# Optimization experiments

Measured on AMD Instinct MI355X. Metric: run time of the kernel, lower is better.

Reference implementation:

```python
import jax, jax.numpy as jnp
import numpy as np

M, N, DIM, BATCH = 64, 64, 256, 4096
GRID = M * N
ALPHA = 0.5
SIGMA = float(np.sqrt(M * N) / 2.0)  # 32.0, default sigma


def _grid_locations():
    ii, jj = np.meshgrid(np.arange(M), np.arange(N), indexing='ij')
    return np.stack([ii.ravel(), jj.ravel()], axis=1).astype(np.int64)  # [GRID, 2]


def _grid_distance_mat(locs):
    # non-periodic: squared euclidean distance between grid locations
    d = locs[:, None, :].astype(np.float32) - locs[None, :, :].astype(np.float32)
    return (d ** 2).sum(-1).astype(np.float32)  # [GRID, GRID]


def setup_inputs() -> dict:
    key = jax.random.key(0)
    k1, k2 = jax.random.split(key)
    locs = _grid_locations()
    return {
        'x': jax.random.normal(k1, (BATCH, DIM), dtype=jnp.float32),
        'centroids': jax.random.normal(k2, (GRID, DIM), dtype=jnp.float32),
        'distance_mat': jnp.asarray(_grid_distance_mat(locs)),
        'locations': jnp.asarray(locs),
        'learning_rate_op': jnp.ones((), dtype=jnp.float32),
    }


def reference(x, centroids, distance_mat, locations, learning_rate_op):
    B = x.shape[0]
    # cdist(x, centroids) with p=2: [B, GRID]
    d2 = ((x ** 2).sum(-1, keepdims=True)
          + (centroids ** 2).sum(-1)[None, :]
          - 2.0 * x @ centroids.T)
    dists = jnp.sqrt(jnp.maximum(d2, 0.0))
    bmu_index = jnp.argmin(dists, axis=-1)            # [B]
    mindist = jnp.min(dists, axis=-1)                 # [B]
    bmu_loc = locations[bmu_index]                    # [B, 2]

    alpha_op = ALPHA * learning_rate_op
    sigma_op = SIGMA * learning_rate_op
    bmu_dist_sq = distance_mat[bmu_index]             # gather rows: [B, GRID]
    neighbourhood = jnp.exp(-bmu_dist_sq / (2.0 * sigma_op ** 2 + 1e-5))
    lrm = alpha_op * neighbourhood                    # [B, GRID]

    # delta = mean_b lrm[b,g] * (x[b,d] - centroids[g,d]), factored to avoid [B,GRID,DIM]
    delta = (lrm.T @ x) / B - jnp.mean(lrm, axis=0)[:, None] * centroids
    new_centroids = centroids + delta
    return new_centroids, bmu_loc, jnp.mean(mindist)
```

## Files before the change

### kernel.cpp

```cpp
#include <hip/hip_runtime.h>
#include <cstdint>
#include <cstddef>

#define DIM    256
#define BATCH  4096
#define GRID_N 4096
#define STEPS  12

typedef _Float16 f16x8 __attribute__((ext_vector_type(8)));
typedef _Float16 f16x4 __attribute__((ext_vector_type(4)));
typedef float    f32x4 __attribute__((ext_vector_type(4)));

#define OFF_APK  0u
#define OFF_S    0u
#define OFF_BPK  1048576u
#define OFF_CNT  1048576u
#define OFF_U    1052672u
#define OFF_GX   2101248u
#define OFF_WCNT 2105344u
#define OFF_XN   2109440u
#define OFF_CN   2113536u
#define OFF_MD   2117632u
#define OFF_PV   2121728u
#define OFF_PI   2252800u

#define OUT_BMU  1048576u
#define OUT_MD   1056768u

__device__ __forceinline__ void load_lds16(const void* g, void* l) {
  __builtin_amdgcn_global_load_lds(
      (const __attribute__((address_space(1))) unsigned int*)g,
      (__attribute__((address_space(3))) unsigned int*)l, 16, 0, 0);
}

__global__ __launch_bounds__(256) void packnorm_kernel(
    const float* __restrict__ x, const float* __restrict__ cen,
    const float* __restrict__ lr,
    _Float16* __restrict__ Apk, _Float16* __restrict__ Bpk,
    float* __restrict__ xn, float* __restrict__ cn, float* __restrict__ Gx) {
  int row  = blockIdx.x * 4 + (threadIdx.x >> 6);
  int lane = threadIdx.x & 63;
  bool isx = row < BATCH;
  const float* src = isx ? (x + (size_t)row * DIM)
                         : (cen + (size_t)(row - BATCH) * DIM);
  float4 v = *(const float4*)(src + lane * 4);

  _Float16 h0 = (_Float16)v.x, h1 = (_Float16)v.y,
           h2 = (_Float16)v.z, h3 = (_Float16)v.w;
  _Float16 l0 = (_Float16)(v.x - (float)h0), l1 = (_Float16)(v.y - (float)h1),
           l2 = (_Float16)(v.z - (float)h2), l3 = (_Float16)(v.w - (float)h3);

  _Float16* dst = (isx ? Apk : Bpk) + (size_t)(isx ? row : row - BATCH) * 512;
  *(f16x4*)(dst + lane * 4)       = (f16x4){h0, h1, h2, h3};
  *(f16x4*)(dst + 256 + lane * 4) = (f16x4){l0, l1, l2, l3};

  float s = v.x * v.x + v.y * v.y + v.z * v.z + v.w * v.w;
#pragma unroll
  for (int off = 32; off >= 1; off >>= 1) s += __shfl_xor(s, off);
  if (lane == 0) {
    if (isx) xn[row] = s;
    else     cn[row - BATCH] = s;
  }

  if (blockIdx.x == 0) {
    float sg  = 32.f * lr[0];
    float inv = 1.f / (2.f * sg * sg + 1e-5f);
#pragma unroll
    for (int i = 0; i < 16; ++i) {
      int g = i * 256 + threadIdx.x;
      float d = (float)((g >> 6) - (g & 63));
      Gx[g] = expf(-d * d * inv);
    }
  }
}

__global__ __launch_bounds__(256) void gemm_argmin_kernel(
    const _Float16* __restrict__ Apk, const _Float16* __restrict__ Bpk,
    const float* __restrict__ cnorm, float* __restrict__ pv, int* __restrict__ pi) {
  __shared__ __align__(16) _Float16 lds[2][2][8192];
  const int tid  = threadIdx.x;
  const int lane = tid & 63, w = tid >> 6;
  const int wr = w >> 1, wc = w & 1;
  const int row0 = blockIdx.y * 128, col0 = blockIdx.x * 128;
  const int t15 = lane & 15, q = lane >> 4;
  const int sw  = t15 & 7;
  const int srow   = w * 32 + (lane >> 3);
  const int schunk = (lane & 7) ^ ((lane >> 3) & 7);

  f32x4 acc[4][4];
#pragma unroll
  for (int m = 0; m < 4; ++m)
#pragma unroll
    for (int n = 0; n < 4; ++n) acc[m][n] = (f32x4){0.f, 0.f, 0.f, 0.f};

  auto STAGE = [&](int b, int step) {
    const int seg = step >> 2, k = (step & 3) << 6;
    const int aoff = ((seg == 2) ? 256 : 0) + k;
    const int boff = ((seg == 1) ? 256 : 0) + k;
    const _Float16* Ab = Apk + (size_t)(row0 + srow) * 512 + aoff + schunk * 8;
    const _Float16* Bb = Bpk + (size_t)(col0 + srow) * 512 + boff + schunk * 8;
    _Float16* Al = &lds[b][0][w * 2048];
    _Float16* Bl = &lds[b][1][w * 2048];
#pragma unroll
    for (int i = 0; i < 4; ++i) {
      load_lds16(Ab + (size_t)i * 8 * 512, Al + i * 512);
      load_lds16(Bb + (size_t)i * 8 * 512, Bl + i * 512);
    }
  };

  STAGE(0, 0);
  for (int t = 0; t < STEPS; ++t) {
    const int b = t & 1;
    __syncthreads();
    if (t + 1 < STEPS) STAGE(b ^ 1, t + 1);
#pragma unroll
    for (int kk = 0; kk < 2; ++kk) {
      f16x8 af[4], bf[4];
#pragma unroll
      for (int m = 0; m < 4; ++m) {
        int r = wr * 64 + m * 16 + t15;
        af[m] = *(const f16x8*)&lds[b][0][r * 64 + (((kk * 4 + q) ^ sw) * 8)];
      }
#pragma unroll
      for (int n = 0; n < 4; ++n) {
        int r = wc * 64 + n * 16 + t15;
        bf[n] = *(const f16x8*)&lds[b][1][r * 64 + (((kk * 4 + q) ^ sw) * 8)];
      }
#pragma unroll
      for (int m = 0; m < 4; ++m)
#pragma unroll
        for (int n = 0; n < 4; ++n)
          acc[m][n] = __builtin_amdgcn_mfma_f32_16x16x32_f16(af[m], bf[n], acc[m][n], 0, 0, 0);
    }
  }
  __syncthreads();

  float cnv[4];
#pragma unroll
  for (int n = 0; n < 4; ++n) cnv[n] = cnorm[col0 + wc * 64 + n * 16 + t15];

  float* cv = (float*)&lds[0][0][0];
  int*   ci = (int*)&lds[0][1][0];
#pragma unroll
  for (int m = 0; m < 4; ++m) {
#pragma unroll
    for (int reg = 0; reg < 4; ++reg) {
      float bv = 1e30f; int bi = 0x7fffffff;
#pragma unroll
      for (int n = 0; n < 4; ++n) {
        float v = cnv[n] - 2.f * acc[m][n][reg];
        if (v < bv) { bv = v; bi = col0 + wc * 64 + n * 16 + t15; }
      }
#pragma unroll
      for (int off = 1; off < 16; off <<= 1) {
        float ov = __shfl_xor(bv, off);
        int   oi = __shfl_xor(bi, off);
        if (ov < bv || (ov == bv && oi < bi)) { bv = ov; bi = oi; }
      }
      if (t15 == 0) {
        int r = wr * 64 + m * 16 + q * 4 + reg;
        cv[r * 2 + wc] = bv;
        ci[r * 2 + wc] = bi;
      }
    }
  }
  __syncthreads();
  if (tid < 128) {
    float v0 = cv[tid * 2];     int i0 = ci[tid * 2];
    float v1 = cv[tid * 2 + 1]; int i1 = ci[tid * 2 + 1];
    if (v1 < v0 || (v1 == v0 && i1 < i0)) { v0 = v1; i0 = i1; }
    pv[(size_t)(row0 + tid) * 32 + blockIdx.x] = v0;
    pi[(size_t)(row0 + tid) * 32 + blockIdx.x] = i0;
  }
}

__global__ __launch_bounds__(256) void finalize_kernel(
    const float* __restrict__ pv, const int* __restrict__ pi,
    const float* __restrict__ xn, const float* __restrict__ x,
    float* __restrict__ S, float* __restrict__ cnt,
    float* __restrict__ md, float* __restrict__ out) {
  const int w = threadIdx.x >> 6, l = threadIdx.x & 63;
  const int b = blockIdx.x * 4 + w;
  float v = pv[(size_t)b * 32 + (l & 31)];
  int idx  = pi[(size_t)b * 32 + (l & 31)];
#pragma unroll
  for (int off = 16; off >= 1; off >>= 1) {
    float ov = __shfl_xor(v, off);
    int   oi = __shfl_xor(idx, off);
    if (ov < v || (ov == v && oi < idx)) { v = ov; idx = oi; }
  }
  if (l == 0) {
    md[b] = sqrtf(fmaxf(xn[b] + v, 0.f));
    out[OUT_BMU + (size_t)b * 2 + 0] = (float)(idx >> 6);
    out[OUT_BMU + (size_t)b * 2 + 1] = (float)(idx & 63);
    atomicAdd(cnt + idx, 1.f);
  }
#pragma unroll
  for (int c = 0; c < 4; ++c)
    atomicAdd(S + (size_t)idx * DIM + c * 64 + l, x[(size_t)b * DIM + c * 64 + l]);
}

__global__ __launch_bounds__(256) void wcnt_kernel(const float* __restrict__ cnt,
                                                   const float* __restrict__ Gx,
                                                   const float* __restrict__ md,
                                                   float* __restrict__ Wcnt,
                                                   float* __restrict__ out) {
  __shared__ float cs[4096], gs[4096], inner[4096];
  const int t = threadIdx.x;
  for (int i = 0; i < 16; i++) { cs[i * 256 + t] = cnt[i * 256 + t]; gs[i * 256 + t] = Gx[i * 256 + t]; }
  __syncthreads();
  for (int i = 0; i < 16; i++) {
    int idx = i * 256 + t; int ki = idx >> 6, gj = idx & 63;
    float a = 0.f;
    for (int kj = 0; kj < 64; kj++) a += gs[kj * 64 + gj] * cs[ki * 64 + kj];
    inner[idx] = a;
  }
  __syncthreads();
  const int g = blockIdx.x * 256 + t, gi = g >> 6, gj = g & 63;
  float a = 0.f;
  for (int ki = 0; ki < 64; ki++) a += gs[gi * 64 + ki] * inner[ki * 64 + gj];
  Wcnt[g] = a;

  if (blockIdx.x == 0) {
    float s = 0.f;
#pragma unroll
    for (int i = 0; i < 16; i++) s += md[i * 256 + t];
#pragma unroll
    for (int off = 32; off >= 1; off >>= 1) s += __shfl_xor(s, off);
    __shared__ float wsum[4];
    if ((t & 63) == 0) wsum[t >> 6] = s;
    __syncthreads();
    if (t == 0) out[OUT_MD] = (wsum[0] + wsum[1] + wsum[2] + wsum[3]) * (1.f / (float)BATCH);
  }
}

__global__ __launch_bounds__(256) void e1_kernel(const float* __restrict__ S,
                                                 const float* __restrict__ Gx,
                                                 float* __restrict__ U) {
  __shared__ float Ss[4096];
  const int t = threadIdx.x, dd = t & 63, gq = t >> 6;
  const int kj = blockIdx.x >> 2, dq = blockIdx.x & 3;
#pragma unroll 4
  for (int i = 0; i < 16; ++i) {
    int ki = i * 4 + gq;
    Ss[ki * 64 + dd] = S[((size_t)ki * 64 + kj) * 256 + dq * 64 + dd];
  }
  __syncthreads();
  float a[16];
#pragma unroll
  for (int gg = 0; gg < 16; ++gg) a[gg] = 0.f;
  for (int ki = 0; ki < 64; ++ki) {
    float s = Ss[ki * 64 + dd];
#pragma unroll
    for (int gg = 0; gg < 16; ++gg)
      a[gg] += Gx[ki * 64 + gq * 16 + gg] * s;
  }
#pragma unroll
  for (int gg = 0; gg < 16; ++gg)
    U[((size_t)(gq * 16 + gg) * 64 + kj) * 256 + dq * 64 + dd] = a[gg];
}

__global__ __launch_bounds__(256) void e2_kernel(const float* __restrict__ U,
                                                 const float* __restrict__ Gx,
                                                 const float* __restrict__ Wcnt,
                                                 const float* __restrict__ cen,
                                                 const float* __restrict__ lr,
                                                 float* __restrict__ out) {
  __shared__ float Us[4096];
  const int t = threadIdx.x, dd = t & 63, gq = t >> 6;
  const int gi = blockIdx.x >> 2, dq = blockIdx.x & 3;
#pragma unroll 4
  for (int i = 0; i < 16; ++i) {
    int kj = i * 4 + gq;
    Us[kj * 64 + dd] = U[((size_t)gi * 64 + kj) * 256 + dq * 64 + dd];
  }
  __syncthreads();
  float a[16];
#pragma unroll
  for (int gg = 0; gg < 16; ++gg) a[gg] = 0.f;
  for (int kj = 0; kj < 64; ++kj) {
    float s = Us[kj * 64 + dd];
#pragma unroll
    for (int gg = 0; gg < 16; ++gg)
      a[gg] += Gx[kj * 64 + gq * 16 + gg] * s;
  }
  const float coef = 0.5f * lr[0] / (float)BATCH;
#pragma unroll
  for (int gg = 0; gg < 16; ++gg) {
    int g = gi * 64 + gq * 16 + gg;
    float c = cen[(size_t)g * 256 + dq * 64 + dd];
    out[(size_t)g * 256 + dq * 64 + dd] = c + coef * (a[gg] - Wcnt[g] * c);
  }
}

extern "C" void kernel_launch(void* const* d_in, const int* in_sizes, int n_in,
                              void* d_out, int out_size, void* d_ws, size_t ws_size,
                              hipStream_t stream) {
  const float* x   = (const float*)d_in[0];
  const float* cen = (const float*)d_in[1];
  const float* lr  = (const float*)d_in[4];
  float* out = (float*)d_out;
  float* ws  = (float*)d_ws;

  _Float16* Apk = (_Float16*)(ws + OFF_APK);
  _Float16* Bpk = (_Float16*)(ws + OFF_BPK);
  float* S    = ws + OFF_S;
  float* cnt  = ws + OFF_CNT;
  float* U    = ws + OFF_U;
  float* Gx   = ws + OFF_GX;
  float* Wcnt = ws + OFF_WCNT;
  float* xn   = ws + OFF_XN;
  float* cnw  = ws + OFF_CN;
  float* md   = ws + OFF_MD;
  float* pv   = ws + OFF_PV;
  int*   pi   = (int*)(ws + OFF_PI);

  packnorm_kernel<<<2048, 256, 0, stream>>>(x, cen, lr, Apk, Bpk, xn, cnw, Gx);
  gemm_argmin_kernel<<<dim3(32, 32), 256, 0, stream>>>(Apk, Bpk, cnw, pv, pi);
  hipMemsetAsync(S, 0, (size_t)(1048576 + 4096) * sizeof(float), stream);
  finalize_kernel<<<1024, 256, 0, stream>>>(pv, pi, xn, x, S, cnt, md, out);
  wcnt_kernel<<<16, 256, 0, stream>>>(cnt, Gx, md, Wcnt, out);
  e1_kernel<<<256, 256, 0, stream>>>(S, Gx, U);
  e2_kernel<<<256, 256, 0, stream>>>(U, Gx, Wcnt, cen, lr, out);
}
```

Measured before the change: 187.3 us.

## Fuse all SOM stages into one cooperative persistent kernel with grid syncs

Replaces the chain of six kernel launches and a memset with a single cooperative kernel of 512 blocks that runs packing, the fp16-split GEMM with argmin, zeroing, scatter-accumulation, the separable neighbourhood passes and the final update, separated by grid.sync barriers. Each block now handles several tiles that previously took separate blocks. The aim is to remove launch gaps and the memset. The cost is that 512 blocks give less parallelism in the GEMM phase than the 1024-block grid did, and the grid barriers add overhead. If the cooperative launch fails, it falls back to the old multi-kernel path.

```diff
diff --git a/kernel.cpp b/kernel.cpp
--- a/kernel.cpp
+++ b/kernel.cpp
@@ -1,10 +1,12 @@
 #include <hip/hip_runtime.h>
+#include <hip/hip_cooperative_groups.h>
 #include <cstdint>
 #include <cstddef>
 
+namespace cg = cooperative_groups;
+
 #define DIM    256
 #define BATCH  4096
-#define GRID_N 4096
 #define STEPS  12
 
 typedef _Float16 f16x8 __attribute__((ext_vector_type(8)));
@@ -14,15 +16,15 @@
 #define OFF_APK  0u
 #define OFF_S    0u
 #define OFF_BPK  1048576u
-#define OFF_CNT  1048576u
-#define OFF_U    1052672u
-#define OFF_GX   2101248u
-#define OFF_WCNT 2105344u
-#define OFF_XN   2109440u
-#define OFF_CN   2113536u
-#define OFF_MD   2117632u
-#define OFF_PV   2121728u
-#define OFF_PI   2252800u
+#define OFF_U    1048576u
+#define OFF_GX   2097152u
+#define OFF_XN   2101248u
+#define OFF_CN   2105344u
+#define OFF_MD   2109440u
+#define OFF_WCNT 2113536u
+#define OFF_PV   2117632u
+#define OFF_PI   2248704u
+#define OFF_CNT  2379776u
 
 #define OUT_BMU  1048576u
 #define OUT_MD   1056768u
@@ -31,6 +33,285 @@
   __builtin_amdgcn_global_load_lds(
       (const __attribute__((address_space(1))) unsigned int*)g,
       (__attribute__((address_space(3))) unsigned int*)l, 16, 0, 0);
+}
+
+__global__ __launch_bounds__(256, 2) void som_mega(
+    const float* __restrict__ x, const float* __restrict__ cen,
+    const float* __restrict__ lr, float* __restrict__ ws,
+    float* __restrict__ out) {
+  cg::grid_group grid = cg::this_grid();
+  __shared__ __align__(16) unsigned char smem[65536];
+
+  const int bid  = blockIdx.x;
+  const int tid  = threadIdx.x;
+  const int lane = tid & 63;
+  const int w    = tid >> 6;
+
+  _Float16* Apk = (_Float16*)(ws + OFF_APK);
+  _Float16* Bpk = (_Float16*)(ws + OFF_BPK);
+  float* S    = ws + OFF_S;
+  float* U    = ws + OFF_U;
+  float* Gx   = ws + OFF_GX;
+  float* xn   = ws + OFF_XN;
+  float* cnw  = ws + OFF_CN;
+  float* md   = ws + OFF_MD;
+  float* Wcnt = ws + OFF_WCNT;
+  float* pv   = ws + OFF_PV;
+  int*   pi   = (int*)(ws + OFF_PI);
+  float* cnt  = ws + OFF_CNT;
+
+  {
+#pragma unroll
+    for (int pass = 0; pass < 4; ++pass) {
+      int row = bid * 16 + pass * 4 + w;
+      bool isx = row < BATCH;
+      const float* src = isx ? (x + (size_t)row * DIM)
+                             : (cen + (size_t)(row - BATCH) * DIM);
+      float4 v = *(const float4*)(src + lane * 4);
+      _Float16 h0 = (_Float16)v.x, h1 = (_Float16)v.y,
+               h2 = (_Float16)v.z, h3 = (_Float16)v.w;
+      _Float16 l0 = (_Float16)(v.x - (float)h0), l1 = (_Float16)(v.y - (float)h1),
+               l2 = (_Float16)(v.z - (float)h2), l3 = (_Float16)(v.w - (float)h3);
+      _Float16* dst = (isx ? Apk : Bpk) + (size_t)(isx ? row : row - BATCH) * 512;
+      *(f16x4*)(dst + lane * 4)       = (f16x4){h0, h1, h2, h3};
+      *(f16x4*)(dst + 256 + lane * 4) = (f16x4){l0, l1, l2, l3};
+      float s = v.x * v.x + v.y * v.y + v.z * v.z + v.w * v.w;
+#pragma unroll
+      for (int off = 32; off >= 1; off >>= 1) s += __shfl_xor(s, off);
+      if (lane == 0) { if (isx) xn[row] = s; else cnw[row - BATCH] = s; }
+    }
+    if (bid == 0) {
+      float sg  = 32.f * lr[0];
+      float inv = 1.f / (2.f * sg * sg + 1e-5f);
+#pragma unroll
+      for (int i = 0; i < 16; ++i) {
+        int g = i * 256 + tid;
+        float d = (float)((g >> 6) - (g & 63));
+        Gx[g] = expf(-d * d * inv);
+      }
+    } else if (bid == 1) {
+      float4 z = {0.f, 0.f, 0.f, 0.f};
+#pragma unroll
+      for (int i = 0; i < 4; ++i) ((float4*)cnt)[i * 256 + tid] = z;
+    }
+  }
+  grid.sync();
+
+  {
+    auto lds = (_Float16(*)[2][8192])smem;
+    const int wr = w >> 1, wc = w & 1;
+    const int by = bid >> 4, bxp = bid & 15;
+    const int row0 = by * 128;
+    const int t15 = lane & 15, q = lane >> 4;
+    const int swz = t15 & 7;
+    const int srow = w * 32 + (lane >> 3);
+    const int schunk = (lane & 7) ^ ((lane >> 3) & 7);
+
+    for (int tt = 0; tt < 2; ++tt) {
+      const int bx = bxp * 2 + tt;
+      const int col0 = bx * 128;
+      f32x4 acc[4][4];
+#pragma unroll
+      for (int m = 0; m < 4; ++m)
+#pragma unroll
+        for (int n = 0; n < 4; ++n) acc[m][n] = (f32x4){0.f, 0.f, 0.f, 0.f};
+
+      auto STAGE = [&](int b, int step) {
+        const int seg = step >> 2, k = (step & 3) << 6;
+        const int aoff = ((seg == 2) ? 256 : 0) + k;
+        const int boff = ((seg == 1) ? 256 : 0) + k;
+        const _Float16* Ab = Apk + (size_t)(row0 + srow) * 512 + aoff + schunk * 8;
+        const _Float16* Bb = Bpk + (size_t)(col0 + srow) * 512 + boff + schunk * 8;
+        _Float16* Al = &lds[b][0][w * 2048];
+        _Float16* Bl = &lds[b][1][w * 2048];
+#pragma unroll
+        for (int i = 0; i < 4; ++i) {
+          load_lds16(Ab + (size_t)i * 8 * 512, Al + i * 512);
+          load_lds16(Bb + (size_t)i * 8 * 512, Bl + i * 512);
+        }
+      };
+
+      STAGE(0, 0);
+      for (int t = 0; t < STEPS; ++t) {
+        const int b = t & 1;
+        __syncthreads();
+        if (t + 1 < STEPS) STAGE(b ^ 1, t + 1);
+#pragma unroll
+        for (int kk = 0; kk < 2; ++kk) {
+          f16x8 af[4], bf[4];
+#pragma unroll
+          for (int m = 0; m < 4; ++m) {
+            int r = wr * 64 + m * 16 + t15;
+            af[m] = *(const f16x8*)&lds[b][0][r * 64 + (((kk * 4 + q) ^ swz) * 8)];
+          }
+#pragma unroll
+          for (int n = 0; n < 4; ++n) {
+            int r = wc * 64 + n * 16 + t15;
+            bf[n] = *(const f16x8*)&lds[b][1][r * 64 + (((kk * 4 + q) ^ swz) * 8)];
+          }
+#pragma unroll
+          for (int m = 0; m < 4; ++m)
+#pragma unroll
+            for (int n = 0; n < 4; ++n)
+              acc[m][n] = __builtin_amdgcn_mfma_f32_16x16x32_f16(af[m], bf[n], acc[m][n], 0, 0, 0);
+        }
+      }
+      __syncthreads();
+
+      float cnv[4];
+#pragma unroll
+      for (int n = 0; n < 4; ++n) cnv[n] = cnw[col0 + wc * 64 + n * 16 + t15];
+
+      float* cv = (float*)smem;
+      int*   ci = (int*)(smem + 16384);
+#pragma unroll
+      for (int m = 0; m < 4; ++m) {
+#pragma unroll
+        for (int reg = 0; reg < 4; ++reg) {
+          float bv = 1e30f; int bi = 0x7fffffff;
+#pragma unroll
+          for (int n = 0; n < 4; ++n) {
+            float v = cnv[n] - 2.f * acc[m][n][reg];
+            if (v < bv) { bv = v; bi = col0 + wc * 64 + n * 16 + t15; }
+          }
+#pragma unroll
+          for (int off = 1; off < 16; off <<= 1) {
+            float ov = __shfl_xor(bv, off);
+            int   oi = __shfl_xor(bi, off);
+            if (ov < bv || (ov == bv && oi < bi)) { bv = ov; bi = oi; }
+          }
+          if (t15 == 0) {
+            int r = wr * 64 + m * 16 + q * 4 + reg;
+            cv[r * 2 + wc] = bv;
+            ci[r * 2 + wc] = bi;
+          }
+        }
+      }
+      __syncthreads();
+      if (tid < 128) {
+        float v0 = cv[tid * 2];     int i0 = ci[tid * 2];
+        float v1 = cv[tid * 2 + 1]; int i1 = ci[tid * 2 + 1];
+        if (v1 < v0 || (v1 == v0 && i1 < i0)) { v0 = v1; i0 = i1; }
+        pv[(size_t)(row0 + tid) * 32 + bx] = v0;
+        pi[(size_t)(row0 + tid) * 32 + bx] = i0;
+      }
+      __syncthreads();
+    }
+  }
+  grid.sync();
+
+  {
+    float4 z = {0.f, 0.f, 0.f, 0.f};
+    float4* S4 = (float4*)S;
+    S4[bid * 512 + tid] = z;
+    S4[bid * 512 + 256 + tid] = z;
+  }
+  grid.sync();
+
+  {
+#pragma unroll
+    for (int i = 0; i < 2; ++i) {
+      int b = bid * 8 + w * 2 + i;
+      float v = pv[(size_t)b * 32 + (lane & 31)];
+      int idx  = pi[(size_t)b * 32 + (lane & 31)];
+#pragma unroll
+      for (int off = 16; off >= 1; off >>= 1) {
+        float ov = __shfl_xor(v, off);
+        int   oi = __shfl_xor(idx, off);
+        if (ov < v || (ov == v && oi < idx)) { v = ov; idx = oi; }
+      }
+      if (lane == 0) {
+        md[b] = sqrtf(fmaxf(xn[b] + v, 0.f));
+        out[OUT_BMU + (size_t)b * 2 + 0] = (float)(idx >> 6);
+        out[OUT_BMU + (size_t)b * 2 + 1] = (float)(idx & 63);
+        atomicAdd(cnt + idx, 1.f);
+      }
+#pragma unroll
+      for (int c = 0; c < 4; ++c)
+        atomicAdd(S + (size_t)idx * DIM + c * 64 + lane,
+                  x[(size_t)b * DIM + c * 64 + lane]);
+    }
+  }
+  grid.sync();
+
+  if (bid < 256) {
+    float* Ss = (float*)smem;
+    const int dd = lane, gq = w;
+    const int kj = bid >> 2, dq = bid & 3;
+    for (int i = 0; i < 16; ++i) {
+      int ki = i * 4 + gq;
+      Ss[ki * 64 + dd] = S[((size_t)ki * 64 + kj) * 256 + dq * 64 + dd];
+    }
+    __syncthreads();
+    float a[16];
+#pragma unroll
+    for (int gg = 0; gg < 16; ++gg) a[gg] = 0.f;
+    for (int ki = 0; ki < 64; ++ki) {
+      float s = Ss[ki * 64 + dd];
+#pragma unroll
+      for (int gg = 0; gg < 16; ++gg)
+        a[gg] += Gx[ki * 64 + gq * 16 + gg] * s;
+    }
+#pragma unroll
+    for (int gg = 0; gg < 16; ++gg)
+      U[((size_t)(gq * 16 + gg) * 64 + kj) * 256 + dq * 64 + dd] = a[gg];
+  } else if (bid < 272) {
+    float* cs = (float*)smem;
+    float* gs = cs + 4096;
+    float* inner = gs + 4096;
+    const int t = tid;
+    for (int i = 0; i < 16; i++) { cs[i * 256 + t] = cnt[i * 256 + t]; gs[i * 256 + t] = Gx[i * 256 + t]; }
+    __syncthreads();
+    for (int i = 0; i < 16; i++) {
+      int idx = i * 256 + t; int ki = idx >> 6, gj = idx & 63;
+      float a = 0.f;
+      for (int kj2 = 0; kj2 < 64; kj2++) a += gs[kj2 * 64 + gj] * cs[ki * 64 + kj2];
+      inner[idx] = a;
+    }
+    __syncthreads();
+    const int g = (bid - 256) * 256 + t, gi = g >> 6, gj = g & 63;
+    float a = 0.f;
+    for (int ki = 0; ki < 64; ki++) a += gs[gi * 64 + ki] * inner[ki * 64 + gj];
+    Wcnt[g] = a;
+  } else if (bid == 272) {
+    float s = 0.f;
+#pragma unroll
+    for (int i = 0; i < 16; i++) s += md[i * 256 + tid];
+#pragma unroll
+    for (int off = 32; off >= 1; off >>= 1) s += __shfl_xor(s, off);
+    float* wsum = (float*)smem;
+    if (lane == 0) wsum[w] = s;
+    __syncthreads();
+    if (tid == 0) out[OUT_MD] = (wsum[0] + wsum[1] + wsum[2] + wsum[3]) * (1.f / (float)BATCH);
+  }
+  grid.sync();
+
+  if (bid < 256) {
+    float* Us = (float*)smem;
+    const int dd = lane, gq = w;
+    const int gi = bid >> 2, dq = bid & 3;
+    for (int i = 0; i < 16; ++i) {
+      int kj = i * 4 + gq;
+      Us[kj * 64 + dd] = U[((size_t)gi * 64 + kj) * 256 + dq * 64 + dd];
+    }
+    __syncthreads();
+    float a[16];
+#pragma unroll
+    for (int gg = 0; gg < 16; ++gg) a[gg] = 0.f;
+    for (int kj = 0; kj < 64; ++kj) {
+      float s = Us[kj * 64 + dd];
+#pragma unroll
+      for (int gg = 0; gg < 16; ++gg)
+        a[gg] += Gx[kj * 64 + gq * 16 + gg] * s;
+    }
+    const float coef = 0.5f * lr[0] / (float)BATCH;
+#pragma unroll
+    for (int gg = 0; gg < 16; ++gg) {
+      int g = gi * 64 + gq * 16 + gg;
+      float c = cen[(size_t)g * 256 + dq * 64 + dd];
+      out[(size_t)g * 256 + dq * 64 + dd] = c + coef * (a[gg] - Wcnt[g] * c);
+    }
+  }
 }
 
 __global__ __launch_bounds__(256) void packnorm_kernel(
@@ -44,24 +325,17 @@
   const float* src = isx ? (x + (size_t)row * DIM)
                          : (cen + (size_t)(row - BATCH) * DIM);
   float4 v = *(const float4*)(src + lane * 4);
-
   _Float16 h0 = (_Float16)v.x, h1 = (_Float16)v.y,
            h2 = (_Float16)v.z, h3 = (_Float16)v.w;
   _Float16 l0 = (_Float16)(v.x - (float)h0), l1 = (_Float16)(v.y - (float)h1),
            l2 = (_Float16)(v.z - (float)h2), l3 = (_Float16)(v.w - (float)h3);
-
   _Float16* dst = (isx ? Apk : Bpk) + (size_t)(isx ? row : row - BATCH) * 512;
   *(f16x4*)(dst + lane * 4)       = (f16x4){h0, h1, h2, h3};
   *(f16x4*)(dst + 256 + lane * 4) = (f16x4){l0, l1, l2, l3};
-
   float s = v.x * v.x + v.y * v.y + v.z * v.z + v.w * v.w;
 #pragma unroll
   for (int off = 32; off >= 1; off >>= 1) s += __shfl_xor(s, off);
-  if (lane == 0) {
-    if (isx) xn[row] = s;
-    else     cn[row - BATCH] = s;
-  }
-
+  if (lane == 0) { if (isx) xn[row] = s; else cn[row - BATCH] = s; }
   if (blockIdx.x == 0) {
     float sg  = 32.f * lr[0];
     float inv = 1.f / (2.f * sg * sg + 1e-5f);
@@ -220,7 +494,6 @@
   float a = 0.f;
   for (int ki = 0; ki < 64; ki++) a += gs[gi * 64 + ki] * inner[ki * 64 + gj];
   Wcnt[g] = a;
-
   if (blockIdx.x == 0) {
     float s = 0.f;
 #pragma unroll
@@ -305,21 +578,27 @@
   _Float16* Apk = (_Float16*)(ws + OFF_APK);
   _Float16* Bpk = (_Float16*)(ws + OFF_BPK);
   float* S    = ws + OFF_S;
-  float* cnt  = ws + OFF_CNT;
   float* U    = ws + OFF_U;
   float* Gx   = ws + OFF_GX;
-  float* Wcnt = ws + OFF_WCNT;
   float* xn   = ws + OFF_XN;
   float* cnw  = ws + OFF_CN;
   float* md   = ws + OFF_MD;
+  float* Wcnt = ws + OFF_WCNT;
   float* pv   = ws + OFF_PV;
   int*   pi   = (int*)(ws + OFF_PI);
-
-  packnorm_kernel<<<2048, 256, 0, stream>>>(x, cen, lr, Apk, Bpk, xn, cnw, Gx);
-  gemm_argmin_kernel<<<dim3(32, 32), 256, 0, stream>>>(Apk, Bpk, cnw, pv, pi);
-  hipMemsetAsync(S, 0, (size_t)(1048576 + 4096) * sizeof(float), stream);
-  finalize_kernel<<<1024, 256, 0, stream>>>(pv, pi, xn, x, S, cnt, md, out);
-  wcnt_kernel<<<16, 256, 0, stream>>>(cnt, Gx, md, Wcnt, out);
-  e1_kernel<<<256, 256, 0, stream>>>(S, Gx, U);
-  e2_kernel<<<256, 256, 0, stream>>>(U, Gx, Wcnt, cen, lr, out);
-}
+  float* cnt  = ws + OFF_CNT;
+
+  void* args[] = { (void*)&x, (void*)&cen, (void*)&lr, (void*)&ws, (void*)&out };
+  hipError_t err = hipLaunchCooperativeKernel((const void*)som_mega, dim3(512),
+                                              dim3(256), args, 0, stream);
+  if (err != hipSuccess) {
+    packnorm_kernel<<<2048, 256, 0, stream>>>(x, cen, lr, Apk, Bpk, xn, cnw, Gx);
+    gemm_argmin_kernel<<<dim3(32, 32), 256, 0, stream>>>(Apk, Bpk, cnw, pv, pi);
+    hipMemsetAsync(S, 0, (size_t)1048576 * sizeof(float), stream);
+    hipMemsetAsync(cnt, 0, (size_t)4096 * sizeof(float), stream);
+    finalize_kernel<<<1024, 256, 0, stream>>>(pv, pi, xn, x, S, cnt, md, out);
+    wcnt_kernel<<<16, 256, 0, stream>>>(cnt, Gx, md, Wcnt, out);
+    e1_kernel<<<256, 256, 0, stream>>>(S, Gx, U);
+    e2_kernel<<<256, 256, 0, stream>>>(U, Gx, Wcnt, cen, lr, out);
+  }
+}
```

Result: slower. 481.7 us (+157.2%).

## Fuse wcnt into e1 launch and single-buffer GEMM LDS staging

Applied to the files above, without the earlier changes.

Merges the wcnt kernel and the mean-distance reduction into the e1 kernel as extra blocks (273 blocks total), removing one launch and letting the small Wcnt work run concurrently with the U computation. Separately, the GEMM argmin kernel drops LDS double buffering: each step now loads a tile, syncs, then computes, halving LDS use to raise occupancy. The cost is that global-to-LDS loads no longer overlap MFMA work within a block, and the e1 launch now mixes blocks of very different shape and shared-memory size, which may reduce its occupancy.

```diff
diff --git a/kernel.cpp b/kernel.cpp
--- a/kernel.cpp
+++ b/kernel.cpp
@@ -4,7 +4,6 @@
 
 #define DIM    256
 #define BATCH  4096
-#define GRID_N 4096
 #define STEPS  12
 
 typedef _Float16 f16x8 __attribute__((ext_vector_type(8)));
@@ -44,24 +43,17 @@
   const float* src = isx ? (x + (size_t)row * DIM)
                          : (cen + (size_t)(row - BATCH) * DIM);
   float4 v = *(const float4*)(src + lane * 4);
-
   _Float16 h0 = (_Float16)v.x, h1 = (_Float16)v.y,
            h2 = (_Float16)v.z, h3 = (_Float16)v.w;
   _Float16 l0 = (_Float16)(v.x - (float)h0), l1 = (_Float16)(v.y - (float)h1),
            l2 = (_Float16)(v.z - (float)h2), l3 = (_Float16)(v.w - (float)h3);
-
   _Float16* dst = (isx ? Apk : Bpk) + (size_t)(isx ? row : row - BATCH) * 512;
   *(f16x4*)(dst + lane * 4)       = (f16x4){h0, h1, h2, h3};
   *(f16x4*)(dst + 256 + lane * 4) = (f16x4){l0, l1, l2, l3};
-
   float s = v.x * v.x + v.y * v.y + v.z * v.z + v.w * v.w;
 #pragma unroll
   for (int off = 32; off >= 1; off >>= 1) s += __shfl_xor(s, off);
-  if (lane == 0) {
-    if (isx) xn[row] = s;
-    else     cn[row - BATCH] = s;
-  }
-
+  if (lane == 0) { if (isx) xn[row] = s; else cn[row - BATCH] = s; }
   if (blockIdx.x == 0) {
     float sg  = 32.f * lr[0];
     float inv = 1.f / (2.f * sg * sg + 1e-5f);
@@ -77,7 +69,7 @@
 __global__ __launch_bounds__(256) void gemm_argmin_kernel(
     const _Float16* __restrict__ Apk, const _Float16* __restrict__ Bpk,
     const float* __restrict__ cnorm, float* __restrict__ pv, int* __restrict__ pi) {
-  __shared__ __align__(16) _Float16 lds[2][2][8192];
+  __shared__ __align__(16) _Float16 lds[2][8192];
   const int tid  = threadIdx.x;
   const int lane = tid & 63, w = tid >> 6;
   const int wr = w >> 1, wc = w & 1;
@@ -93,38 +85,35 @@
 #pragma unroll
     for (int n = 0; n < 4; ++n) acc[m][n] = (f32x4){0.f, 0.f, 0.f, 0.f};
 
-  auto STAGE = [&](int b, int step) {
-    const int seg = step >> 2, k = (step & 3) << 6;
-    const int aoff = ((seg == 2) ? 256 : 0) + k;
-    const int boff = ((seg == 1) ? 256 : 0) + k;
-    const _Float16* Ab = Apk + (size_t)(row0 + srow) * 512 + aoff + schunk * 8;
-    const _Float16* Bb = Bpk + (size_t)(col0 + srow) * 512 + boff + schunk * 8;
-    _Float16* Al = &lds[b][0][w * 2048];
-    _Float16* Bl = &lds[b][1][w * 2048];
-#pragma unroll
-    for (int i = 0; i < 4; ++i) {
-      load_lds16(Ab + (size_t)i * 8 * 512, Al + i * 512);
-      load_lds16(Bb + (size_t)i * 8 * 512, Bl + i * 512);
-    }
-  };
-
-  STAGE(0, 0);
   for (int t = 0; t < STEPS; ++t) {
-    const int b = t & 1;
-    __syncthreads();
-    if (t + 1 < STEPS) STAGE(b ^ 1, t + 1);
+    if (t) __syncthreads();
+    {
+      const int seg = t >> 2, k = (t & 3) << 6;
+      const int aoff = ((seg == 2) ? 256 : 0) + k;
+      const int boff = ((seg == 1) ? 256 : 0) + k;
+      const _Float16* Ab = Apk + (size_t)(row0 + srow) * 512 + aoff + schunk * 8;
+      const _Float16* Bb = Bpk + (size_t)(col0 + srow) * 512 + boff + schunk * 8;
+      _Float16* Al = &lds[0][w * 2048];
+      _Float16* Bl = &lds[1][w * 2048];
+#pragma unroll
+      for (int i = 0; i < 4; ++i) {
+        load_lds16(Ab + (size_t)i * 8 * 512, Al + i * 512);
+        load_lds16(Bb + (size_t)i * 8 * 512, Bl + i * 512);
+      }
+    }
+    __syncthreads();
 #pragma unroll
     for (int kk = 0; kk < 2; ++kk) {
       f16x8 af[4], bf[4];
 #pragma unroll
       for (int m = 0; m < 4; ++m) {
         int r = wr * 64 + m * 16 + t15;
-        af[m] = *(const f16x8*)&lds[b][0][r * 64 + (((kk * 4 + q) ^ sw) * 8)];
+        af[m] = *(const f16x8*)&lds[0][r * 64 + (((kk * 4 + q) ^ sw) * 8)];
       }
 #pragma unroll
       for (int n = 0; n < 4; ++n) {
         int r = wc * 64 + n * 16 + t15;
-        bf[n] = *(const f16x8*)&lds[b][1][r * 64 + (((kk * 4 + q) ^ sw) * 8)];
+        bf[n] = *(const f16x8*)&lds[1][r * 64 + (((kk * 4 + q) ^ sw) * 8)];
       }
 #pragma unroll
       for (int m = 0; m < 4; ++m)
@@ -139,8 +128,8 @@
 #pragma unroll
   for (int n = 0; n < 4; ++n) cnv[n] = cnorm[col0 + wc * 64 + n * 16 + t15];
 
-  float* cv = (float*)&lds[0][0][0];
-  int*   ci = (int*)&lds[0][1][0];
+  float* cv = (float*)&lds[0][0];
+  int*   ci = (int*)&lds[1][0];
 #pragma unroll
   for (int m = 0; m < 4; ++m) {
 #pragma unroll
@@ -200,64 +189,64 @@
     atomicAdd(S + (size_t)idx * DIM + c * 64 + l, x[(size_t)b * DIM + c * 64 + l]);
 }
 
-__global__ __launch_bounds__(256) void wcnt_kernel(const float* __restrict__ cnt,
-                                                   const float* __restrict__ Gx,
-                                                   const float* __restrict__ md,
-                                                   float* __restrict__ Wcnt,
-                                                   float* __restrict__ out) {
-  __shared__ float cs[4096], gs[4096], inner[4096];
-  const int t = threadIdx.x;
-  for (int i = 0; i < 16; i++) { cs[i * 256 + t] = cnt[i * 256 + t]; gs[i * 256 + t] = Gx[i * 256 + t]; }
-  __syncthreads();
-  for (int i = 0; i < 16; i++) {
-    int idx = i * 256 + t; int ki = idx >> 6, gj = idx & 63;
-    float a = 0.f;
-    for (int kj = 0; kj < 64; kj++) a += gs[kj * 64 + gj] * cs[ki * 64 + kj];
-    inner[idx] = a;
-  }
-  __syncthreads();
-  const int g = blockIdx.x * 256 + t, gi = g >> 6, gj = g & 63;
-  float a = 0.f;
-  for (int ki = 0; ki < 64; ki++) a += gs[gi * 64 + ki] * inner[ki * 64 + gj];
-  Wcnt[g] = a;
-
-  if (blockIdx.x == 0) {
-    float s = 0.f;
-#pragma unroll
-    for (int i = 0; i < 16; i++) s += md[i * 256 + t];
-#pragma unroll
-    for (int off = 32; off >= 1; off >>= 1) s += __shfl_xor(s, off);
-    __shared__ float wsum[4];
-    if ((t & 63) == 0) wsum[t >> 6] = s;
-    __syncthreads();
-    if (t == 0) out[OUT_MD] = (wsum[0] + wsum[1] + wsum[2] + wsum[3]) * (1.f / (float)BATCH);
-  }
-}
-
 __global__ __launch_bounds__(256) void e1_kernel(const float* __restrict__ S,
                                                  const float* __restrict__ Gx,
-                                                 float* __restrict__ U) {
-  __shared__ float Ss[4096];
-  const int t = threadIdx.x, dd = t & 63, gq = t >> 6;
-  const int kj = blockIdx.x >> 2, dq = blockIdx.x & 3;
+                                                 const float* __restrict__ cnt,
+                                                 const float* __restrict__ md,
+                                                 float* __restrict__ U,
+                                                 float* __restrict__ Wcnt,
+                                                 float* __restrict__ out) {
+  __shared__ float smem[12288];
+  const int bid = blockIdx.x, tid = threadIdx.x;
+  if (bid < 256) {
+    float* Ss = smem;
+    const int dd = tid & 63, gq = tid >> 6;
+    const int kj = bid >> 2, dq = bid & 3;
 #pragma unroll 4
-  for (int i = 0; i < 16; ++i) {
-    int ki = i * 4 + gq;
-    Ss[ki * 64 + dd] = S[((size_t)ki * 64 + kj) * 256 + dq * 64 + dd];
-  }
-  __syncthreads();
-  float a[16];
-#pragma unroll
-  for (int gg = 0; gg < 16; ++gg) a[gg] = 0.f;
-  for (int ki = 0; ki < 64; ++ki) {
-    float s = Ss[ki * 64 + dd];
+    for (int i = 0; i < 16; ++i) {
+      int ki = i * 4 + gq;
+      Ss[ki * 64 + dd] = S[((size_t)ki * 64 + kj) * 256 + dq * 64 + dd];
+    }
+    __syncthreads();
+    float a[16];
+#pragma unroll
+    for (int gg = 0; gg < 16; ++gg) a[gg] = 0.f;
+    for (int ki = 0; ki < 64; ++ki) {
+      float s = Ss[ki * 64 + dd];
+#pragma unroll
+      for (int gg = 0; gg < 16; ++gg)
+        a[gg] += Gx[ki * 64 + gq * 16 + gg] * s;
+    }
 #pragma unroll
     for (int gg = 0; gg < 16; ++gg)
-      a[gg] += Gx[ki * 64 + gq * 16 + gg] * s;
-  }
-#pragma unroll
-  for (int gg = 0; gg < 16; ++gg)
-    U[((size_t)(gq * 16 + gg) * 64 + kj) * 256 + dq * 64 + dd] = a[gg];
+      U[((size_t)(gq * 16 + gg) * 64 + kj) * 256 + dq * 64 + dd] = a[gg];
+  } else if (bid < 272) {
+    float* cs = smem;
+    float* gs = smem + 4096;
+    float* inner = smem + 8192;
+    for (int i = 0; i < 16; i++) { cs[i * 256 + tid] = cnt[i * 256 + tid]; gs[i * 256 + tid] = Gx[i * 256 + tid]; }
+    __syncthreads();
+    for (int i = 0; i < 16; i++) {
+      int idx = i * 256 + tid; int ki = idx >> 6, gj = idx & 63;
+      float a = 0.f;
+      for (int kj = 0; kj < 64; kj++) a += gs[kj * 64 + gj] * cs[ki * 64 + kj];
+      inner[idx] = a;
+    }
+    __syncthreads();
+    const int g = (bid - 256) * 256 + tid, gi = g >> 6, gj = g & 63;
+    float a = 0.f;
+    for (int ki = 0; ki < 64; ki++) a += gs[gi * 64 + ki] * inner[ki * 64 + gj];
+    Wcnt[g] = a;
+  } else {
+    float s = 0.f;
+#pragma unroll
+    for (int i = 0; i < 16; i++) s += md[i * 256 + tid];
+#pragma unroll
+    for (int off = 32; off >= 1; off >>= 1) s += __shfl_xor(s, off);
+    if ((tid & 63) == 0) smem[tid >> 6] = s;
+    __syncthreads();
+    if (tid == 0) out[OUT_MD] = (smem[0] + smem[1] + smem[2] + smem[3]) * (1.f / (float)BATCH);
+  }
 }
 
 __global__ __launch_bounds__(256) void e2_kernel(const float* __restrict__ U,
@@ -319,7 +308,6 @@
   gemm_argmin_kernel<<<dim3(32, 32), 256, 0, stream>>>(Apk, Bpk, cnw, pv, pi);
   hipMemsetAsync(S, 0, (size_t)(1048576 + 4096) * sizeof(float), stream);
   finalize_kernel<<<1024, 256, 0, stream>>>(pv, pi, xn, x, S, cnt, md, out);
-  wcnt_kernel<<<16, 256, 0, stream>>>(cnt, Gx, md, Wcnt, out);
-  e1_kernel<<<256, 256, 0, stream>>>(S, Gx, U);
+  e1_kernel<<<273, 256, 0, stream>>>(S, Gx, cnt, md, U, Wcnt, out);
   e2_kernel<<<256, 256, 0, stream>>>(U, Gx, Wcnt, cen, lr, out);
 }
```

After: 181.1 us. -3.3%, faster.
